# Kernel optimization log

Hardware: AMD Instinct MI355X
Metric: run time of the kernel (lower is better)

The kernel has to match this reference:

```python
import jax, jax.numpy as jnp
import numpy as np

N, D, H, C, ED, E = 50000, 128, 8, 16, 16, 800000  # nodes, model dim, heads, head dim, edge dim, edges

def _layer_norm(x, g, b, eps=1e-5):
    mu = x.mean(-1, keepdims=True)
    var = ((x - mu) ** 2).mean(-1, keepdims=True)
    return (x - mu) * jax.lax.rsqrt(var + eps) * g + b

def setup_inputs() -> dict:
    key = jax.random.key(0)
    ks = jax.random.split(key, 24)
    s = 0.05
    inp = {
        'x': jax.random.normal(ks[0], (N, D), jnp.float32),
        'edge_index': jax.random.randint(ks[1], (2, E), 0, N, jnp.int32),
        'edge_attr': jax.random.normal(ks[2], (E, ED), jnp.float32),
        # TransformerConv params (Linear convention: y = x @ W + b)
        'wq': s * jax.random.normal(ks[3], (D, H * C)), 'bq': s * jax.random.normal(ks[4], (H * C,)),
        'wk': s * jax.random.normal(ks[5], (D, H * C)), 'bk': s * jax.random.normal(ks[6], (H * C,)),
        'wv': s * jax.random.normal(ks[7], (D, H * C)), 'bv': s * jax.random.normal(ks[8], (H * C,)),
        'we': s * jax.random.normal(ks[9], (ED, H * C)),            # lin_edge, bias=False
        'wskip': s * jax.random.normal(ks[10], (D, H * C)), 'bskip': s * jax.random.normal(ks[11], (H * C,)),
        'wbeta': s * jax.random.normal(ks[12], (3 * H * C, 1)),     # lin_beta, bias=False
        # norms
        'ln1_g': 1.0 + s * jax.random.normal(ks[13], (D,)), 'ln1_b': s * jax.random.normal(ks[14], (D,)),
        'ln2_g': 1.0 + s * jax.random.normal(ks[15], (D,)), 'ln2_b': s * jax.random.normal(ks[16], (D,)),
        # FFN
        'w1': s * jax.random.normal(ks[17], (D, 2 * D)), 'b1': s * jax.random.normal(ks[18], (2 * D,)),
        'w2': s * jax.random.normal(ks[19], (2 * D, D)), 'b2': s * jax.random.normal(ks[20], (D,)),
    }
    return inp

def reference(x, edge_index, edge_attr, wq, bq, wk, bk, wv, bv, we, wskip, bskip, wbeta,
              ln1_g, ln1_b, ln2_g, ln2_b, w1, b1, w2, b2):
    src, dst = edge_index[0], edge_index[1]  # message flows src (j) -> dst (i)
    # --- pre-norm + TransformerConv (beta=True, concat=True, eval-mode dropout=identity) ---
    xn = _layer_norm(x, ln1_g, ln1_b)
    q = (xn @ wq + bq).reshape(N, H, C)
    k = (xn @ wk + bk).reshape(N, H, C)
    v = (xn @ wv + bv).reshape(N, H, C)
    e = (edge_attr @ we).reshape(E, H, C)
    kj = k[src] + e                                     # [E,H,C]
    alpha = (q[dst] * kj).sum(-1) / jnp.sqrt(jnp.float32(C))  # [E,H]
    # segment softmax over incoming edges per destination node
    m = jax.ops.segment_max(alpha, dst, num_segments=N)        # [N,H]
    ea = jnp.exp(alpha - m[dst])
    denom = jax.ops.segment_sum(ea, dst, num_segments=N)
    alpha = ea / (denom[dst] + 1e-16)
    msg = (v[src] + e) * alpha[..., None]               # [E,H,C]
    out = jax.ops.segment_sum(msg, dst, num_segments=N).reshape(N, H * C)
    # beta-gated skip
    x_r = xn @ wskip + bskip
    beta = jax.nn.sigmoid(jnp.concatenate([out, x_r, out - x_r], axis=-1) @ wbeta)  # [N,1]
    out = beta * x_r + (1.0 - beta) * out
    x = x + out
    # --- pre-norm FFN ---
    h = _layer_norm(x, ln2_g, ln2_b)
    h = jax.nn.gelu(h @ w1 + b1, approximate=False) @ w2 + b2
    return x + h
```

## Files before the change

### kernel.cpp

```cpp
#include <hip/hip_runtime.h>
#include <math.h>

#define N_NODES 50000
#define D_MODEL 128
#define N_HEADS 8
#define HEAD_C 16
#define E_DIM 16
#define N_EDGES 800000

typedef __attribute__((ext_vector_type(8))) short bf16x8;
typedef __attribute__((ext_vector_type(4))) float f32x4;

__device__ inline ushort f2bf(float f) {
    unsigned u = __float_as_uint(f);
    unsigned r = (u + 0x7fffu + ((u >> 16) & 1u)) >> 16;
    return (ushort)r;
}
__device__ inline float bf2f(ushort h) { return __uint_as_float(((unsigned)h) << 16); }
__device__ inline uint pack2(float a, float b) {
    return (uint)f2bf(a) | ((uint)f2bf(b) << 16);
}

__global__ void prep_weights(const float* __restrict__ wq, const float* __restrict__ wk,
                             const float* __restrict__ wv, const float* __restrict__ wsk,
                             const float* __restrict__ bq, const float* __restrict__ bk,
                             const float* __restrict__ bv, const float* __restrict__ bsk,
                             const float* __restrict__ w1, const float* __restrict__ w2,
                             ushort* __restrict__ wqkvsT, float* __restrict__ bqkvs,
                             ushort* __restrict__ w1T, ushort* __restrict__ w2T)
{
    int idx = blockIdx.x * 256 + threadIdx.x;
    {
        int m = idx >> 7, kk = idx & 127;
        int b = m >> 7, ch = m & 127;
        const float* src = (b == 0) ? wq : (b == 1) ? wk : (b == 2) ? wv : wsk;
        wqkvsT[idx] = f2bf(src[kk * 128 + ch]);
    }
    if (idx < 256 * 128) {
        int m = idx >> 7, k = idx & 127;
        w1T[idx] = f2bf(w1[k * 256 + m]);
    }
    if (idx < 128 * 256) {
        int m = idx >> 8, k = idx & 255;
        w2T[idx] = f2bf(w2[k * 128 + m]);
    }
    if (idx < 512) {
        int b = idx >> 7, ch = idx & 127;
        const float* bb = (b == 0) ? bq : (b == 1) ? bk : (b == 2) ? bv : bsk;
        bqkvs[idx] = bb[ch];
    }
}

__global__ void ln_kernel(const float* __restrict__ in, const float* __restrict__ g,
                          const float* __restrict__ b, ushort* __restrict__ out, int n)
{
    int node = blockIdx.x * 4 + (threadIdx.x >> 6);
    int lane = threadIdx.x & 63;
    if (node >= n) return;
    size_t base = (size_t)node * D_MODEL;
    float v0 = in[base + lane];
    float v1 = in[base + lane + 64];
    float s  = v0 + v1;
    float ss = v0 * v0 + v1 * v1;
    #pragma unroll
    for (int off = 32; off > 0; off >>= 1) {
        s  += __shfl_xor(s,  off, 64);
        ss += __shfl_xor(ss, off, 64);
    }
    float mu  = s * (1.0f / 128.0f);
    float var = ss * (1.0f / 128.0f) - mu * mu;
    float rs  = rsqrtf(var + 1e-5f);
    out[base + lane]      = f2bf((v0 - mu) * rs * g[lane]      + b[lane]);
    out[base + lane + 64] = f2bf((v1 - mu) * rs * g[lane + 64] + b[lane + 64]);
}

__global__ __launch_bounds__(256) void mfma_gemm(
    const ushort* __restrict__ A, const ushort* __restrict__ WT,
    const float* __restrict__ bias, const float* __restrict__ addsrc,
    void* __restrict__ Y, int nrows, int K, int M, int act, int outf32)
{
    __shared__ __align__(16) ushort Al[128 * 128];
    __shared__ __align__(16) ushort Wl[64 * 128];
    int tid = threadIdx.x;
    int wv = tid >> 6, lane = tid & 63;
    int row0 = blockIdx.x * 128;
    int col0 = blockIdx.y * 64;

    f32x4 acc[2][4];
    #pragma unroll
    for (int i = 0; i < 2; ++i)
        #pragma unroll
        for (int j = 0; j < 4; ++j) acc[i][j] = (f32x4){0.f, 0.f, 0.f, 0.f};

    for (int kc = 0; kc < K; kc += 128) {
        __syncthreads();
        #pragma unroll
        for (int i = 0; i < 8; ++i) {
            int c = tid + i * 256;
            int r = c >> 4, c16 = c & 15;
            int gr = row0 + r;
            ulonglong2 val = {0ull, 0ull};
            if (gr < nrows) val = *(const ulonglong2*)(A + (size_t)gr * K + kc + c16 * 8);
            int byte = r * 256 + ((c16 * 16) ^ ((r & 7) << 4));
            *(ulonglong2*)((char*)Al + byte) = val;
        }
        #pragma unroll
        for (int i = 0; i < 4; ++i) {
            int c = tid + i * 256;
            int r = c >> 4, c16 = c & 15;
            ulonglong2 val = *(const ulonglong2*)(WT + (size_t)(col0 + r) * K + kc + c16 * 8);
            int byte = r * 256 + ((c16 * 16) ^ ((r & 7) << 4));
            *(ulonglong2*)((char*)Wl + byte) = val;
        }
        __syncthreads();
        #pragma unroll
        for (int ks = 0; ks < 4; ++ks) {
            bf16x8 af[2], bfr[4];
            #pragma unroll
            for (int rt = 0; rt < 2; ++rt) {
                int r = wv * 32 + rt * 16 + (lane & 15);
                int byte = r * 256 + ((ks * 64 + (lane >> 4) * 16) ^ ((r & 7) << 4));
                af[rt] = *(const bf16x8*)((const char*)Al + byte);
            }
            #pragma unroll
            for (int ct = 0; ct < 4; ++ct) {
                int r = ct * 16 + (lane & 15);
                int byte = r * 256 + ((ks * 64 + (lane >> 4) * 16) ^ ((r & 7) << 4));
                bfr[ct] = *(const bf16x8*)((const char*)Wl + byte);
            }
            #pragma unroll
            for (int rt = 0; rt < 2; ++rt)
                #pragma unroll
                for (int ct = 0; ct < 4; ++ct)
                    acc[rt][ct] = __builtin_amdgcn_mfma_f32_16x16x32_bf16(
                        af[rt], bfr[ct], acc[rt][ct], 0, 0, 0);
        }
    }
    #pragma unroll
    for (int rt = 0; rt < 2; ++rt) {
        #pragma unroll
        for (int ct = 0; ct < 4; ++ct) {
            int gcol = col0 + ct * 16 + (lane & 15);
            float bv = bias[gcol];
            #pragma unroll
            for (int r = 0; r < 4; ++r) {
                int grow = row0 + wv * 32 + rt * 16 + (lane >> 4) * 4 + r;
                if (grow >= nrows) continue;
                float val = acc[rt][ct][r] + bv;
                if (act == 1)
                    val = 0.5f * val * (1.0f + erff(val * 0.70710678118654752f));
                size_t idx = (size_t)grow * M + gcol;
                if (outf32) {
                    float* Yf = (float*)Y;
                    if (addsrc) val += addsrc[idx];
                    Yf[idx] = val;
                } else {
                    ((ushort*)Y)[idx] = f2bf(val);
                }
            }
        }
    }
}

__global__ void hist_kernel(const int* __restrict__ dst, int* __restrict__ deg)
{
    int e = blockIdx.x * 256 + threadIdx.x;
    if (e < N_EDGES) atomicAdd(&deg[dst[e]], 1);
}

__global__ void scan1_kernel(const int* __restrict__ deg, int* __restrict__ off,
                             int* __restrict__ bsum)
{
    __shared__ int sm[256];
    int i = blockIdx.x * 256 + threadIdx.x;
    int v = (i < N_NODES) ? deg[i] : 0;
    sm[threadIdx.x] = v;
    __syncthreads();
    #pragma unroll
    for (int d = 1; d < 256; d <<= 1) {
        int t = (threadIdx.x >= d) ? sm[threadIdx.x - d] : 0;
        __syncthreads();
        sm[threadIdx.x] += t;
        __syncthreads();
    }
    if (i < N_NODES) off[i] = sm[threadIdx.x] - v;
    if (threadIdx.x == 255) bsum[blockIdx.x] = sm[255];
}

__global__ void scan2_kernel(int* __restrict__ bsum, int nb)
{
    __shared__ int sm[256];
    int v = (threadIdx.x < nb) ? bsum[threadIdx.x] : 0;
    sm[threadIdx.x] = v;
    __syncthreads();
    #pragma unroll
    for (int d = 1; d < 256; d <<= 1) {
        int t = (threadIdx.x >= d) ? sm[threadIdx.x - d] : 0;
        __syncthreads();
        sm[threadIdx.x] += t;
        __syncthreads();
    }
    if (threadIdx.x < nb) bsum[threadIdx.x] = sm[threadIdx.x] - v;
}

__global__ void scan3_kernel(int* __restrict__ off, const int* __restrict__ bsum,
                             int* __restrict__ cursor)
{
    int i = blockIdx.x * 256 + threadIdx.x;
    if (i < N_NODES) {
        int o = off[i] + bsum[blockIdx.x];
        off[i] = o;
        cursor[i] = o;
    }
}

__global__ void scatter_kernel(const int* __restrict__ dst, const int* __restrict__ src,
                               const float* __restrict__ eattr, int* __restrict__ cursor,
                               int* __restrict__ src_s, ushort* __restrict__ eattr_s)
{
    int e = blockIdx.x * 256 + threadIdx.x;
    if (e < N_EDGES) {
        int p = atomicAdd(&cursor[dst[e]], 1);
        src_s[p] = src[e];
        const float4* s4 = (const float4*)(eattr + (size_t)e * E_DIM);
        float4 f0 = s4[0], f1 = s4[1], f2 = s4[2], f3 = s4[3];
        uint4 u0, u1;
        u0.x = pack2(f0.x, f0.y); u0.y = pack2(f0.z, f0.w);
        u0.z = pack2(f1.x, f1.y); u0.w = pack2(f1.z, f1.w);
        u1.x = pack2(f2.x, f2.y); u1.y = pack2(f2.z, f2.w);
        u1.z = pack2(f3.x, f3.y); u1.w = pack2(f3.z, f3.w);
        uint4* d4 = (uint4*)(eattr_s + (size_t)p * E_DIM);
        d4[0] = u0; d4[1] = u1;
    }
}

#define ATTN_STEP(P, S, A0, A1, E0, E1) do {                                         \
    int sv_ = src_s[P];                                                              \
    uint eap_ = *(const uint*)(eattr_s + (size_t)(P) * E_DIM + j2);                  \
    float ea0_ = bf2f((ushort)eap_), ea1_ = bf2f((ushort)(eap_ >> 16));              \
    size_t sb_ = (size_t)sv_ * 512;                                                  \
    uint kp_ = *(const uint*)(qkvs + sb_ + 128 + 2 * lane);                          \
    uint vp_ = *(const uint*)(qkvs + sb_ + 256 + 2 * lane);                          \
    float p_ = q0 * bf2f((ushort)kp_) + q1 * bf2f((ushort)(kp_ >> 16))               \
             + ea0_ * qp0 + ea1_ * qp1;                                              \
    p_ += __shfl_xor(p_, 1, 64);                                                     \
    p_ += __shfl_xor(p_, 2, 64);                                                     \
    p_ += __shfl_xor(p_, 4, 64);                                                     \
    float w_ = __expf(fminf(p_ * 0.25f, 60.f));                                      \
    S  += w_;                                                                        \
    A0 += w_ * bf2f((ushort)vp_);                                                    \
    A1 += w_ * bf2f((ushort)(vp_ >> 16));                                            \
    E0 += w_ * ea0_;                                                                 \
    E1 += w_ * ea1_;                                                                 \
} while (0)

__global__ void node_attn(const ushort* __restrict__ qkvs, const float* __restrict__ x,
                          const float* __restrict__ we, const float* __restrict__ wbeta,
                          const int* __restrict__ off, const int* __restrict__ deg,
                          const int* __restrict__ src_s, const ushort* __restrict__ eattr_s,
                          float* __restrict__ xnew)
{
    __shared__ float wl[E_DIM * 128];
    __shared__ float weT[128 * 17];
    __shared__ float sc4[4][128];
    for (int t = threadIdx.x; t < E_DIM * 32; t += 256)
        *(float4*)&wl[t * 4] = *(const float4*)&we[t * 4];
    for (int t = threadIdx.x; t < E_DIM * 128; t += 256) {
        int j = t >> 7, ch = t & 127;
        weT[ch * 17 + j] = we[t];
    }
    __syncthreads();

    int nl   = threadIdx.x >> 6;
    int node = blockIdx.x * 4 + nl;
    int lane = threadIdx.x & 63;
    if (node >= N_NODES) return;

    int j2 = (lane & 7) * 2;
    int hb = (lane >> 3) * 16;

    size_t nb = (size_t)node * 512;
    uint qp = *(const uint*)(qkvs + nb + 2 * lane);
    float q0 = bf2f((ushort)qp), q1 = bf2f((ushort)(qp >> 16));

    sc4[nl][2 * lane]     = q0;
    sc4[nl][2 * lane + 1] = q1;
    float qp0 = 0.f, qp1 = 0.f;
    #pragma unroll
    for (int c = 0; c < 16; ++c) {
        float qc = sc4[nl][hb + c];
        qp0 += qc * weT[(hb + c) * 17 + j2];
        qp1 += qc * weT[(hb + c) * 17 + j2 + 1];
    }

    float SA = 0.f, A0a = 0.f, A1a = 0.f, E0a = 0.f, E1a = 0.f;
    float SB = 0.f, A0b = 0.f, A1b = 0.f, E0b = 0.f, E1b = 0.f;

    int o = off[node], dg = deg[node];
    int i = 0;
    for (; i + 2 <= dg; i += 2) {
        ATTN_STEP(o + i,     SA, A0a, A1a, E0a, E1a);
        ATTN_STEP(o + i + 1, SB, A0b, A1b, E0b, E1b);
    }
    if (i < dg)
        ATTN_STEP(o + i, SA, A0a, A1a, E0a, E1a);

    float S  = SA + SB;
    float A0 = A0a + A0b, A1 = A1a + A1b;
    float E0 = E0a + E0b, E1 = E1a + E1b;

    sc4[nl][2 * lane]     = E0;
    sc4[nl][2 * lane + 1] = E1;
    float ep0 = 0.f, ep1 = 0.f;
    #pragma unroll
    for (int j = 0; j < 16; ++j) {
        float es = sc4[nl][hb + j];
        ep0 += es * wl[j * 128 + 2 * lane];
        ep1 += es * wl[j * 128 + 2 * lane + 1];
    }

    float rinv = 1.f / (S + 1e-16f);
    float o0 = (A0 + ep0) * rinv;
    float o1 = (A1 + ep1) * rinv;

    uint xrp = *(const uint*)(qkvs + nb + 384 + 2 * lane);
    float xr0 = bf2f((ushort)xrp), xr1 = bf2f((ushort)(xrp >> 16));
    float2 wb0 = *(const float2*)&wbeta[2 * lane];
    float2 wb1 = *(const float2*)&wbeta[128 + 2 * lane];
    float2 wb2 = *(const float2*)&wbeta[256 + 2 * lane];
    float dot = o0 * wb0.x + o1 * wb0.y + xr0 * wb1.x + xr1 * wb1.y
              + (o0 - xr0) * wb2.x + (o1 - xr1) * wb2.y;
    #pragma unroll
    for (int w = 32; w > 0; w >>= 1) dot += __shfl_xor(dot, w, 64);
    float beta = 1.f / (1.f + __expf(-dot));

    size_t xb = (size_t)node * D_MODEL + 2 * lane;
    float2 xv = *(const float2*)&x[xb];
    float2 outv;
    outv.x = xv.x + beta * xr0 + (1.f - beta) * o0;
    outv.y = xv.y + beta * xr1 + (1.f - beta) * o1;
    *(float2*)&xnew[xb] = outv;
}

extern "C" void kernel_launch(void* const* d_in, const int* in_sizes, int n_in,
                              void* d_out, int out_size, void* d_ws, size_t ws_size,
                              hipStream_t stream)
{
    const float* x     = (const float*)d_in[0];
    const int*   eidx  = (const int*)  d_in[1];
    const float* eattr = (const float*)d_in[2];
    const float* wq  = (const float*)d_in[3];  const float* bq  = (const float*)d_in[4];
    const float* wk  = (const float*)d_in[5];  const float* bk  = (const float*)d_in[6];
    const float* wv  = (const float*)d_in[7];  const float* bv  = (const float*)d_in[8];
    const float* we  = (const float*)d_in[9];
    const float* wsk = (const float*)d_in[10]; const float* bsk = (const float*)d_in[11];
    const float* wbeta = (const float*)d_in[12];
    const float* ln1g = (const float*)d_in[13]; const float* ln1b = (const float*)d_in[14];
    const float* ln2g = (const float*)d_in[15]; const float* ln2b = (const float*)d_in[16];
    const float* w1 = (const float*)d_in[17]; const float* b1 = (const float*)d_in[18];
    const float* w2 = (const float*)d_in[19]; const float* b2 = (const float*)d_in[20];
    const int* srcp = eidx;
    const int* dstp = eidx + N_EDGES;
    float* out = (float*)d_out;

    char* w = (char*)d_ws;
    size_t o = 0;
    ushort* qkvs_b  = (ushort*)(w + o);
    ushort* hidden_b = qkvs_b;
    o += (size_t)N_NODES * 512 * 2;
    float* xnew = (float*)(w + o);  o += (size_t)N_NODES * 128 * 4;
    ushort* eattr_s = (ushort*)(w + o); o += (size_t)N_EDGES * E_DIM * 2;
    int* src_s = (int*)(w + o);     o += (size_t)N_EDGES * 4;
    ushort* xn_b = (ushort*)(w + o);
    ushort* h2_b = xn_b;
    o += (size_t)N_NODES * 128 * 2;
    ushort* wqkvsT = (ushort*)(w + o); o += 512 * 128 * 2;
    ushort* w1T    = (ushort*)(w + o); o += 256 * 128 * 2;
    ushort* w2T    = (ushort*)(w + o); o += 128 * 256 * 2;
    float*  bqkvs  = (float*)(w + o);  o += 4096;
    int* deg    = (int*)(w + o); o += 200704;
    int* offb   = (int*)(w + o); o += 200704;
    int* cursor = (int*)(w + o); o += 200704;
    int* bsum   = (int*)(w + o); o += 4096;

    dim3 blk(256);
    dim3 lngrid((N_NODES + 3) / 4);
    const int NB = (N_NODES + 255) / 256;
    const int EB = (N_EDGES + 255) / 256;
    const int GB = (N_NODES + 127) / 128;

    prep_weights<<<dim3(256), blk, 0, stream>>>(wq, wk, wv, wsk, bq, bk, bv, bsk,
                                                w1, w2, wqkvsT, bqkvs, w1T, w2T);
    ln_kernel<<<lngrid, blk, 0, stream>>>(x, ln1g, ln1b, xn_b, N_NODES);
    mfma_gemm<<<dim3(GB, 8), blk, 0, stream>>>(xn_b, wqkvsT, bqkvs, nullptr,
                                               qkvs_b, N_NODES, 128, 512, 0, 0);
    hipMemsetAsync(deg, 0, (size_t)N_NODES * 4, stream);
    hist_kernel<<<dim3(EB), blk, 0, stream>>>(dstp, deg);
    scan1_kernel<<<dim3(NB), blk, 0, stream>>>(deg, offb, bsum);
    scan2_kernel<<<dim3(1), blk, 0, stream>>>(bsum, NB);
    scan3_kernel<<<dim3(NB), blk, 0, stream>>>(offb, bsum, cursor);
    scatter_kernel<<<dim3(EB), blk, 0, stream>>>(dstp, srcp, eattr, cursor, src_s, eattr_s);
    node_attn<<<lngrid, blk, 0, stream>>>(qkvs_b, x, we, wbeta, offb, deg,
                                          src_s, eattr_s, xnew);
    ln_kernel<<<lngrid, blk, 0, stream>>>(xnew, ln2g, ln2b, h2_b, N_NODES);
    mfma_gemm<<<dim3(GB, 4), blk, 0, stream>>>(h2_b, w1T, b1, nullptr,
                                               hidden_b, N_NODES, 128, 256, 1, 0);
    mfma_gemm<<<dim3(GB, 2), blk, 0, stream>>>(hidden_b, w2T, b2, xnew,
                                               out, N_NODES, 256, 128, 0, 1);
}
```

Before: 331.3 us.

## Interleave K/V layout, software-pipeline edge loads, fuse LN2 into attention

Reorders the QKV weight columns so each lane's K and V pairs for a source node sit next to each other, letting one 8-byte load fetch both. Replaces the two-accumulator unrolled edge loop with a single-accumulator loop that prefetches the next edge's source index, edge attributes and K/V before computing the current one. Folds the 1/sqrt(C) scale into q and the edge projection outside the loop. Fuses the second layer norm into the attention kernel's epilogue, removing a separate launch and a reread of xnew. The cost is one fewer independent accumulator chain per step.

Result: slower. 367.8 us (+11.0%).

```diff
diff --git a/kernel.cpp b/kernel.cpp
--- a/kernel.cpp
+++ b/kernel.cpp
@@ -32,8 +32,11 @@
     int idx = blockIdx.x * 256 + threadIdx.x;
     {
         int m = idx >> 7, kk = idx & 127;
-        int b = m >> 7, ch = m & 127;
-        const float* src = (b == 0) ? wq : (b == 1) ? wk : (b == 2) ? wv : wsk;
+        const float* src; int ch;
+        if (m < 128)      { src = wq;  ch = m; }
+        else if (m < 384) { int t = m - 128, l = t >> 2, r = t & 3;
+                            src = (r < 2) ? wk : wv; ch = 2 * l + (r & 1); }
+        else              { src = wsk; ch = m - 384; }
         wqkvsT[idx] = f2bf(src[kk * 128 + ch]);
     }
     if (idx < 256 * 128) {
@@ -45,9 +48,13 @@
         w2T[idx] = f2bf(w2[k * 128 + m]);
     }
     if (idx < 512) {
-        int b = idx >> 7, ch = idx & 127;
-        const float* bb = (b == 0) ? bq : (b == 1) ? bk : (b == 2) ? bv : bsk;
-        bqkvs[idx] = bb[ch];
+        int m = idx;
+        const float* bb; int ch;
+        if (m < 128)      { bb = bq;  ch = m; }
+        else if (m < 384) { int t = m - 128, l = t >> 2, r = t & 3;
+                            bb = (r < 2) ? bk : bv; ch = 2 * l + (r & 1); }
+        else              { bb = bsk; ch = m - 384; }
+        bqkvs[m] = bb[ch];
     }
 }
 
@@ -234,31 +241,27 @@
     }
 }
 
-#define ATTN_STEP(P, S, A0, A1, E0, E1) do {                                         \
-    int sv_ = src_s[P];                                                              \
-    uint eap_ = *(const uint*)(eattr_s + (size_t)(P) * E_DIM + j2);                  \
-    float ea0_ = bf2f((ushort)eap_), ea1_ = bf2f((ushort)(eap_ >> 16));              \
-    size_t sb_ = (size_t)sv_ * 512;                                                  \
-    uint kp_ = *(const uint*)(qkvs + sb_ + 128 + 2 * lane);                          \
-    uint vp_ = *(const uint*)(qkvs + sb_ + 256 + 2 * lane);                          \
-    float p_ = q0 * bf2f((ushort)kp_) + q1 * bf2f((ushort)(kp_ >> 16))               \
+#define ATTN_COMPUTE(KV, EAP) do {                                                   \
+    float ea0_ = bf2f((ushort)(EAP)), ea1_ = bf2f((ushort)((EAP) >> 16));            \
+    float p_ = q0 * bf2f((ushort)(KV).x) + q1 * bf2f((ushort)((KV).x >> 16))         \
              + ea0_ * qp0 + ea1_ * qp1;                                              \
     p_ += __shfl_xor(p_, 1, 64);                                                     \
     p_ += __shfl_xor(p_, 2, 64);                                                     \
     p_ += __shfl_xor(p_, 4, 64);                                                     \
-    float w_ = __expf(fminf(p_ * 0.25f, 60.f));                                      \
+    float w_ = __expf(fminf(p_, 60.f));                                              \
     S  += w_;                                                                        \
-    A0 += w_ * bf2f((ushort)vp_);                                                    \
-    A1 += w_ * bf2f((ushort)(vp_ >> 16));                                            \
+    A0 += w_ * bf2f((ushort)(KV).y);                                                 \
+    A1 += w_ * bf2f((ushort)((KV).y >> 16));                                         \
     E0 += w_ * ea0_;                                                                 \
     E1 += w_ * ea1_;                                                                 \
 } while (0)
 
 __global__ void node_attn(const ushort* __restrict__ qkvs, const float* __restrict__ x,
                           const float* __restrict__ we, const float* __restrict__ wbeta,
+                          const float* __restrict__ ln2g, const float* __restrict__ ln2b,
                           const int* __restrict__ off, const int* __restrict__ deg,
                           const int* __restrict__ src_s, const ushort* __restrict__ eattr_s,
-                          float* __restrict__ xnew)
+                          float* __restrict__ xnew, ushort* __restrict__ h2)
 {
     __shared__ float wl[E_DIM * 128];
     __shared__ float weT[128 * 17];
@@ -281,10 +284,10 @@
 
     size_t nb = (size_t)node * 512;
     uint qp = *(const uint*)(qkvs + nb + 2 * lane);
-    float q0 = bf2f((ushort)qp), q1 = bf2f((ushort)(qp >> 16));
-
-    sc4[nl][2 * lane]     = q0;
-    sc4[nl][2 * lane + 1] = q1;
+    float q0r = bf2f((ushort)qp), q1r = bf2f((ushort)(qp >> 16));
+
+    sc4[nl][2 * lane]     = q0r;
+    sc4[nl][2 * lane + 1] = q1r;
     float qp0 = 0.f, qp1 = 0.f;
     #pragma unroll
     for (int c = 0; c < 16; ++c) {
@@ -292,22 +295,25 @@
         qp0 += qc * weT[(hb + c) * 17 + j2];
         qp1 += qc * weT[(hb + c) * 17 + j2 + 1];
     }
-
-    float SA = 0.f, A0a = 0.f, A1a = 0.f, E0a = 0.f, E1a = 0.f;
-    float SB = 0.f, A0b = 0.f, A1b = 0.f, E0b = 0.f, E1b = 0.f;
-
+    float q0 = q0r * 0.25f, q1 = q1r * 0.25f;
+    qp0 *= 0.25f; qp1 *= 0.25f;
+
+    float S = 0.f, A0 = 0.f, A1 = 0.f, E0 = 0.f, E1 = 0.f;
     int o = off[node], dg = deg[node];
-    int i = 0;
-    for (; i + 2 <= dg; i += 2) {
-        ATTN_STEP(o + i,     SA, A0a, A1a, E0a, E1a);
-        ATTN_STEP(o + i + 1, SB, A0b, A1b, E0b, E1b);
-    }
-    if (i < dg)
-        ATTN_STEP(o + i, SA, A0a, A1a, E0a, E1a);
-
-    float S  = SA + SB;
-    float A0 = A0a + A0b, A1 = A1a + A1b;
-    float E0 = E0a + E0b, E1 = E1a + E1b;
+
+    if (dg > 0) {
+        int sv0 = src_s[o];
+        uint eap0 = *(const uint*)(eattr_s + (size_t)o * E_DIM + j2);
+        uint2 kv0 = *(const uint2*)(qkvs + (size_t)sv0 * 512 + 128 + 4 * lane);
+        for (int i = 1; i < dg; ++i) {
+            int sv1 = src_s[o + i];
+            uint eap1 = *(const uint*)(eattr_s + (size_t)(o + i) * E_DIM + j2);
+            uint2 kv1 = *(const uint2*)(qkvs + (size_t)sv1 * 512 + 128 + 4 * lane);
+            ATTN_COMPUTE(kv0, eap0);
+            kv0 = kv1; eap0 = eap1;
+        }
+        ATTN_COMPUTE(kv0, eap0);
+    }
 
     sc4[nl][2 * lane]     = E0;
     sc4[nl][2 * lane + 1] = E1;
@@ -336,10 +342,25 @@
 
     size_t xb = (size_t)node * D_MODEL + 2 * lane;
     float2 xv = *(const float2*)&x[xb];
-    float2 outv;
-    outv.x = xv.x + beta * xr0 + (1.f - beta) * o0;
-    outv.y = xv.y + beta * xr1 + (1.f - beta) * o1;
-    *(float2*)&xnew[xb] = outv;
+    float ox = xv.x + beta * xr0 + (1.f - beta) * o0;
+    float oy = xv.y + beta * xr1 + (1.f - beta) * o1;
+    *(float2*)&xnew[xb] = make_float2(ox, oy);
+
+    float s2  = ox + oy;
+    float ss2 = ox * ox + oy * oy;
+    #pragma unroll
+    for (int w = 32; w > 0; w >>= 1) {
+        s2  += __shfl_xor(s2,  w, 64);
+        ss2 += __shfl_xor(ss2, w, 64);
+    }
+    float mu  = s2 * (1.0f / 128.0f);
+    float var = ss2 * (1.0f / 128.0f) - mu * mu;
+    float rs  = rsqrtf(var + 1e-5f);
+    float2 g2 = *(const float2*)&ln2g[2 * lane];
+    float2 b2 = *(const float2*)&ln2b[2 * lane];
+    float h0 = (ox - mu) * rs * g2.x + b2.x;
+    float h1 = (oy - mu) * rs * g2.y + b2.y;
+    ((uint*)h2)[(size_t)node * 64 + lane] = pack2(h0, h1);
 }
 
 extern "C" void kernel_launch(void* const* d_in, const int* in_sizes, int n_in,
@@ -400,9 +421,8 @@
     scan2_kernel<<<dim3(1), blk, 0, stream>>>(bsum, NB);
     scan3_kernel<<<dim3(NB), blk, 0, stream>>>(offb, bsum, cursor);
     scatter_kernel<<<dim3(EB), blk, 0, stream>>>(dstp, srcp, eattr, cursor, src_s, eattr_s);
-    node_attn<<<lngrid, blk, 0, stream>>>(qkvs_b, x, we, wbeta, offb, deg,
-                                          src_s, eattr_s, xnew);
-    ln_kernel<<<lngrid, blk, 0, stream>>>(xnew, ln2g, ln2b, h2_b, N_NODES);
+    node_attn<<<lngrid, blk, 0, stream>>>(qkvs_b, x, we, wbeta, ln2g, ln2b,
+                                          offb, deg, src_s, eattr_s, xnew, h2_b);
     mfma_gemm<<<dim3(GB, 4), blk, 0, stream>>>(h2_b, w1T, b1, nullptr,
                                                hidden_b, N_NODES, 128, 256, 1, 0);
     mfma_gemm<<<dim3(GB, 2), blk, 0, stream>>>(hidden_b, w2T, b2, xnew,
```
